# Kernel optimization log

Hardware: AMD Instinct MI355X
Metric: run time of the kernel (lower is better)

Reference implementation:

```python
import jax, jax.numpy as jnp
from jax import lax
import numpy as np

B = 512          # batch
M = 2000         # num_memories
CC = 16          # conv_channel_size
F = CC * 4 * 6 * 6  # 2304 feature size
BN_EPS = 1e-5
COS_EPS = 1e-8
SHRINK_EPS = 0.01


def conv(x, w, b, stride, pad):
    y = lax.conv_general_dilated(x, w, (stride, stride), [(pad, pad), (pad, pad)],
                                 dimension_numbers=('NCHW', 'OIHW', 'NCHW'))
    return y + b[None, :, None, None]


def deconv(x, w, b, stride, pad, out_pad):
    # w is torch ConvTranspose2d layout: (in, out, kh, kw)
    k = w.shape[2]
    w2 = jnp.flip(w, (2, 3)).transpose(1, 0, 2, 3)  # (out, in, kh, kw)
    p = [(k - 1 - pad, k - 1 - pad + out_pad)] * 2
    y = lax.conv_general_dilated(x, w2, (1, 1), p, lhs_dilation=(stride, stride),
                                 dimension_numbers=('NCHW', 'OIHW', 'NCHW'))
    return y + b[None, :, None, None]


def bn(x, g, b):
    # BatchNorm2d in training mode: per-channel batch statistics (biased var)
    m = x.mean((0, 2, 3), keepdims=True)
    v = x.var((0, 2, 3), keepdims=True)
    return g[None, :, None, None] * (x - m) * lax.rsqrt(v + BN_EPS) + b[None, :, None, None]


def setup_inputs() -> dict:
    key = jax.random.key(0)
    ks = jax.random.split(key, 16)
    rn = lambda k, s, sc=0.05: jax.random.normal(k, s, jnp.float32) * sc
    return {
        'x': jax.random.uniform(ks[0], (B, 1, 96, 96), jnp.float32),
        'c1_w': rn(ks[1], (16, 1, 1, 1), 0.3), 'c1_b': jnp.zeros(16),
        'bn1_g': jnp.ones(16), 'bn1_b': jnp.zeros(16),
        'c2_w': rn(ks[2], (32, 16, 3, 3)), 'c2_b': jnp.zeros(32),
        'bn2_g': jnp.ones(32), 'bn2_b': jnp.zeros(32),
        'c3_w': rn(ks[3], (64, 32, 3, 3)), 'c3_b': jnp.zeros(64),
        'bn3_g': jnp.ones(64), 'bn3_b': jnp.zeros(64),
        'c4_w': rn(ks[4], (64, 64, 3, 3)), 'c4_b': jnp.zeros(64),
        'bn4_g': jnp.ones(64), 'bn4_b': jnp.zeros(64),
        'memory': rn(ks[5], (M, F), 0.03),
        'd0_w': rn(ks[6], (64, 64, 3, 3)), 'd0_b': jnp.zeros(64),
        'dbn0_g': jnp.ones(64), 'dbn0_b': jnp.zeros(64),
        'd1_w': rn(ks[7], (64, 32, 3, 3)), 'd1_b': jnp.zeros(32),
        'dbn1_g': jnp.ones(32), 'dbn1_b': jnp.zeros(32),
        'd2_w': rn(ks[8], (32, 16, 2, 2)), 'd2_b': jnp.zeros(16),
        'dbn2_g': jnp.ones(16), 'dbn2_b': jnp.zeros(16),
        'd3_w': rn(ks[9], (16, 1, 2, 2)), 'd3_b': jnp.zeros(1),
    }


def reference(x, c1_w, c1_b, bn1_g, bn1_b, c2_w, c2_b, bn2_g, bn2_b,
              c3_w, c3_b, bn3_g, bn3_b, c4_w, c4_b, bn4_g, bn4_b, memory,
              d0_w, d0_b, dbn0_g, dbn0_b, d1_w, d1_b, dbn1_g, dbn1_b,
              d2_w, d2_b, dbn2_g, dbn2_b, d3_w, d3_b):
    relu = jax.nn.relu
    # Encoder: 96 -> 49 -> 25 -> 13 -> 6
    h = relu(bn(conv(x, c1_w, c1_b, 2, 1), bn1_g, bn1_b))
    h = relu(bn(conv(h, c2_w, c2_b, 2, 1), bn2_g, bn2_b))
    h = relu(bn(conv(h, c3_w, c3_b, 2, 1), bn3_g, bn3_b))
    h = relu(bn(conv(h, c4_w, c4_b, 2, 0), bn4_g, bn4_b))
    z = h.reshape(h.shape[0], -1)  # (B, 2304)

    # Memory addressing: cosine similarity without materializing (B, M, F)
    zn = jnp.linalg.norm(z, axis=1)          # (B,)
    mn = jnp.linalg.norm(memory, axis=1)     # (M,)
    sim = (z @ memory.T) / jnp.maximum(zn[:, None] * mn[None, :], COS_EPS)
    w = jax.nn.softmax(sim, axis=1)
    # Sparse hard-shrink addressing + L1 renorm
    t = 1.0 / memory.shape[0]
    w = relu(w - t) * w / (jnp.abs(w - t) + SHRINK_EPS)
    w = w / jnp.sum(jnp.abs(w), axis=1, keepdims=True)
    z_hat = w @ memory  # (B, F)

    # Decoder: 6 -> 13 -> 25 -> 49 -> 98
    g = z_hat.reshape(-1, 64, 6, 6)
    g = relu(bn(deconv(g, d0_w, d0_b, 2, 0, 0), dbn0_g, dbn0_b))
    g = relu(bn(deconv(g, d1_w, d1_b, 2, 1, 0), dbn1_g, dbn1_b))
    g = relu(bn(deconv(g, d2_w, d2_b, 2, 1, 1), dbn2_g, dbn2_b))
    g = jax.nn.sigmoid(deconv(g, d3_w, d3_b, 2, 0, 0))
    return g
```

## Files before the change

### kernel.cpp

```cpp
#include <hip/hip_runtime.h>
#include <stdint.h>


typedef unsigned short ushort_t;
typedef __bf16 bf16x8 __attribute__((ext_vector_type(8)));
typedef float f32x4 __attribute__((ext_vector_type(4)));

#define DEV static __device__ __forceinline__

DEV ushort_t f2bf(float f){
  union { float f; uint32_t u; } v; v.f = f;
  return (ushort_t)((v.u + 0x7FFFu + ((v.u >> 16) & 1u)) >> 16);
}
DEV float bf2f(ushort_t u){
  union { uint32_t u; float f; } v; v.u = ((uint32_t)u) << 16;
  return v.f;
}

DEV uint32_t affine2(uint32_t rw, const float* ac, int ci, int nch){
  float lo = bf2f((ushort_t)(rw & 0xffffu));
  float hi = bf2f((ushort_t)(rw >> 16));
  lo = fmaxf(fmaf(ac[ci],   lo, ac[nch+ci]),   0.f);
  hi = fmaxf(fmaf(ac[ci+1], hi, ac[nch+ci+1]), 0.f);
  return (uint32_t)f2bf(lo) | ((uint32_t)f2bf(hi) << 16);
}
DEV uint4 stage_chunk(uint4 raw, const float* ac, int ci0, int nch){
  uint4 o;
  o.x = affine2(raw.x, ac, ci0+0, nch);
  o.y = affine2(raw.y, ac, ci0+2, nch);
  o.z = affine2(raw.z, ac, ci0+4, nch);
  o.w = affine2(raw.w, ac, ci0+6, nch);
  return o;
}

#define H_XS   0
#define H_S2   64
#define H_Q2   96
#define H_S3   192
#define H_Q3   256
#define H_S4   448
#define H_Q4   512
#define H_DS0  704
#define H_DQ0  768
#define H_DS1  960
#define H_DQ1  992
#define H_DS2  1088
#define H_DQ2  1104
#define H_ZN   1152
#define H_MN   1664
#define H_BUK  4096
#define NBUK   16
#define BSTRIDE 1280
#define HDR_FLOATS (H_BUK + NBUK*BSTRIDE)

#define OW2 0
#define OW3 5120
#define OW4 23552
#define OD0 60416
#define OD1 97280
#define OD2 115712
#define NWPK 117760

#define SIMSTRIDE 1024000
#define ZHSTRIDE  1179648

DEV float* bkt(float* hdr, int blk){ return hdr + H_BUK + (size_t)(blk & (NBUK-1))*BSTRIDE; }

DEV void coef_lds(const float* __restrict__ hdr, int offS, int offQ,
                  const float* __restrict__ g, const float* __restrict__ be,
                  float* ac, int nch, float invN, int tid){
  if (tid < nch){
    float s = 0.f, q = 0.f;
    #pragma unroll
    for (int k=0;k<NBUK;k++){
      s += hdr[H_BUK + k*BSTRIDE + offS + tid];
      q += hdr[H_BUK + k*BSTRIDE + offQ + tid];
    }
    float m = s*invN;
    float v = q*invN - m*m;
    float a = g[tid]*rsqrtf(v + 1e-5f);
    ac[tid] = a;
    ac[nch+tid] = be[tid] - m*a;
  }
}

__global__ __launch_bounds__(256) void k_xstats(const float* __restrict__ x, float* __restrict__ hdr){
  __shared__ float red[8];
  float s = 0.f, q = 0.f;
  const int total = 512*49*49;
  for (int idx = blockIdx.x*256 + threadIdx.x; idx < total; idx += gridDim.x*256){
    int b = idx / 2401;
    int r = idx - b*2401;
    int i = r / 49, j = r - i*49;
    float v = 0.f;
    if (i > 0 && j > 0) v = x[(size_t)b*9216 + (2*i-1)*96 + (2*j-1)];
    s += v; q += v*v;
  }
  for (int o=32;o;o>>=1){ s += __shfl_down(s,o,64); q += __shfl_down(q,o,64); }
  int w = threadIdx.x>>6;
  if ((threadIdx.x&63)==0){ red[w*2]=s; red[w*2+1]=q; }
  __syncthreads();
  if (threadIdx.x==0){
    float* bk = bkt(hdr, blockIdx.x);
    atomicAdd(&bk[H_XS+0], red[0]+red[2]+red[4]+red[6]);
    atomicAdd(&bk[H_XS+1], red[1]+red[3]+red[5]+red[7]);
  }
}

__global__ __launch_bounds__(256) void k_wprep2(
    const float* __restrict__ c2w, const float* __restrict__ c3w, const float* __restrict__ c4w,
    const float* __restrict__ d0w, const float* __restrict__ d1w, const float* __restrict__ d2w,
    ushort_t* __restrict__ WPK){
  int i = blockIdx.x*256 + threadIdx.x;
  if (i >= NWPK) return;
  float val = 0.f;
  if (i < OW3){
    int co = i/160, k = i - co*160, tap = k>>4, ci = k&15;
    if (tap < 9) val = c2w[(co*16+ci)*9+tap];
  } else if (i < OW4){
    int r = i - OW3; int co = r/288, k = r - co*288, tap = k>>5, ci = k&31;
    val = c3w[(co*32+ci)*9+tap];
  } else if (i < OD0){
    int r = i - OW4; int co = r/576, k = r - co*576, tap = k>>6, ci = k&63;
    val = c4w[(co*64+ci)*9+tap];
  } else if (i < OD1){
    int r = i - OD0;
    const int base[4]={0,16384,24576,32768}, K[4]={256,128,128,64};
    const int T0[4][4] = {{0,2,6,8},{1,7,0,0},{3,5,0,0},{4,0,0,0}};
    int cl = (r<16384)?0:(r<24576)?1:(r<32768)?2:3;
    int rr = r - base[cl]; int co = rr/K[cl], k = rr - co*K[cl], t = k>>6, ci = k&63;
    val = d0w[(ci*64+co)*9 + T0[cl][t]];
  } else if (i < OD2){
    int r = i - OD1;
    const int base[4]={0,2048,6144,10240}, K[4]={64,128,128,256};
    const int T1[4][4] = {{4,0,0,0},{3,5,0,0},{1,7,0,0},{0,2,6,8}};
    int cl = (r<2048)?0:(r<6144)?1:(r<10240)?2:3;
    int rr = r - base[cl]; int co = rr/K[cl], k = rr - co*K[cl], t = k>>6, ci = k&63;
    val = d1w[(ci*32+co)*9 + T1[cl][t]];
  } else {
    int r = i - OD2;
    int cl = r>>9, s = r&511, co = s>>5, ci = s&31;
    const int pis[4]={0,0,1,1}, pjs[4]={0,1,0,1};
    val = d2w[((ci*16+co)*2 + (1-pis[cl]))*2 + (1-pjs[cl])];
  }
  WPK[i] = f2bf(val);
}

__global__ __launch_bounds__(256) void k_memrows(const float* __restrict__ mem, float* __restrict__ hdr,
                                                 ushort_t* __restrict__ mbf){
  __shared__ float red[4];
  const int m = blockIdx.x, tid = threadIdx.x;
  float part = 0.f;
  for (int i=tid;i<2304;i+=256){
    float v = mem[(size_t)m*2304+i];
    mbf[(size_t)m*2304+i] = f2bf(v);
    part += v*v;
  }
  for (int o=32;o;o>>=1) part += __shfl_down(part,o,64);
  if ((tid&63)==0) red[tid>>6] = part;
  __syncthreads();
  if (tid==0) hdr[H_MN+m] = sqrtf(red[0]+red[1]+red[2]+red[3]);
}

__global__ __launch_bounds__(256) void k_memT(const float* __restrict__ mem, ushort_t* __restrict__ mt){
  __shared__ ushort_t tile[32][33];
  const int ft = blockIdx.x % 72, mtile = blockIdx.x / 72;
  const int tx = threadIdx.x & 31, ty = threadIdx.x >> 5;
  #pragma unroll
  for (int r0=0;r0<4;r0++){
    int m = mtile*32 + r0*8 + ty;
    int f = ft*32 + tx;
    float v = (m < 2000) ? mem[(size_t)m*2304 + f] : 0.f;
    tile[r0*8+ty][tx] = f2bf(v);
  }
  __syncthreads();
  #pragma unroll
  for (int r0=0;r0<4;r0++){
    int f = ft*32 + r0*8 + ty;
    mt[(size_t)f*2016 + mtile*32 + tx] = tile[tx][r0*8+ty];
  }
}

__global__ __launch_bounds__(256) void k_conv2m(
    const float* __restrict__ x, const ushort_t* __restrict__ WPK, const float* __restrict__ b2g,
    const float* __restrict__ c1w, const float* __restrict__ c1b,
    const float* __restrict__ bn1g, const float* __restrict__ bn1b,
    float* __restrict__ hdr, ushort_t* __restrict__ out){
  __shared__ ushort_t inp[27*51*16];
  __shared__ float ac[32];
  const int blk = blockIdx.x, b = blk>>1, h = blk&1, tid = threadIdx.x;
  const int ro = h*13, nr = h?12:13, npos = nr*25, ntiles = (npos+15)>>4;
  if (tid < 16){
    float sx=0.f, qx=0.f;
    #pragma unroll
    for (int k=0;k<NBUK;k++){ sx += hdr[H_BUK+k*BSTRIDE+H_XS]; qx += hdr[H_BUK+k*BSTRIDE+H_XS+1]; }
    const float N = 512.f*49.f*49.f;
    float mx = sx/N, vx = qx/N - mx*mx;
    float mean = c1w[tid]*mx + c1b[tid];
    float a = bn1g[tid]*rsqrtf(c1w[tid]*c1w[tid]*vx + 1e-5f);
    ac[tid] = a*c1w[tid];
    ac[16+tid] = a*(c1b[tid]-mean) + bn1b[tid];
  }
  __syncthreads();
  for (int e = tid; e < 27*51; e += 256){
    int lr = e/51, gc = e - lr*51;
    int grg = 2*ro + lr;
    bool inside = (grg>=1 && grg<=49 && gc>=1 && gc<=49);
    float v = 0.f;
    if (grg>=2 && grg<=49 && gc>=2 && gc<=49) v = x[(size_t)b*9216 + (2*grg-3)*96 + (2*gc-3)];
    ushort_t hv[16];
    if (inside){
      #pragma unroll
      for (int c=0;c<16;c++) hv[c] = f2bf(fmaxf(fmaf(ac[c], v, ac[16+c]), 0.f));
    } else {
      #pragma unroll
      for (int c=0;c<16;c++) hv[c] = 0;
    }
    uint32_t w0[8];
    #pragma unroll
    for (int c=0;c<8;c++) w0[c] = (uint32_t)hv[2*c] | ((uint32_t)hv[2*c+1]<<16);
    uint4* dst = (uint4*)&inp[e*16];
    dst[0] = make_uint4(w0[0],w0[1],w0[2],w0[3]);
    dst[1] = make_uint4(w0[4],w0[5],w0[6],w0[7]);
  }
  __syncthreads();
  const int wv = tid>>6, lane = tid&63, r = lane&15, q = lane>>4;
  const int cotile = wv&1;
  bf16x8 af[5];
  #pragma unroll
  for (int c=0;c<5;c++) af[c] = *(const bf16x8*)(WPK + OW2 + (cotile*16+r)*160 + c*32 + q*8);
  float biasr[4];
  #pragma unroll
  for (int v=0;v<4;v++) biasr[v] = b2g[cotile*16 + q*4 + v];
  const int TOFF[10] = {0,1,2,51,52,53,102,103,104,0};
  const int qhi = q>>1, ci0 = (q&1)*8;
  float sacc[4]={0,0,0,0}, qacc[4]={0,0,0,0};
  for (int t = wv>>1; t < ntiles; t += 2){
    int p = t*16 + r;
    bool ok = p < npos;
    int pc = ok ? p : 0;
    int a_ = pc/25, c_ = pc - a_*25;
    int pb = (2*a_)*51 + 2*c_;
    f32x4 acc = {0.f,0.f,0.f,0.f};
    #pragma unroll
    for (int c=0;c<5;c++){
      int toff = qhi ? TOFF[2*c+1] : TOFF[2*c];
      bf16x8 bv = *(const bf16x8*)&inp[(pb + toff)*16 + ci0];
      acc = __builtin_amdgcn_mfma_f32_16x16x32_bf16(af[c], bv, acc, 0, 0, 0);
    }
    if (ok){
      int pg = (ro + a_)*25 + c_;
      ushort_t pk[4];
      #pragma unroll
      for (int reg=0;reg<4;reg++){
        float y = acc[reg] + biasr[reg];
        pk[reg] = f2bf(y);
        sacc[reg] += y; qacc[reg] += y*y;
      }
      *(uint2*)&out[((size_t)b*625 + pg)*32 + cotile*16 + q*4] =
        make_uint2((uint32_t)pk[0] | ((uint32_t)pk[1]<<16), (uint32_t)pk[2] | ((uint32_t)pk[3]<<16));
    }
  }
  float* bk = bkt(hdr, blk);
  #pragma unroll
  for (int reg=0;reg<4;reg++){
    float s = sacc[reg], qq = qacc[reg];
    for (int o=8;o;o>>=1){ s += __shfl_down(s,o,16); qq += __shfl_down(qq,o,16); }
    if (r==0){ atomicAdd(&bk[H_S2+cotile*16+q*4+reg], s); atomicAdd(&bk[H_Q2+cotile*16+q*4+reg], qq); }
  }
}

__global__ __launch_bounds__(256) void k_conv3m(
    const ushort_t* __restrict__ h2, const ushort_t* __restrict__ WPK, const float* __restrict__ b3g,
    const float* __restrict__ g, const float* __restrict__ be,
    float* __restrict__ hdr, ushort_t* __restrict__ out){
  __shared__ ushort_t inp[15*27*32];
  __shared__ float ac[64];
  const int blk = blockIdx.x, b = blk>>1, h = blk&1, tid = threadIdx.x;
  const int a0 = h*7, na = h?6:7, npos = na*13, ntiles = (npos+15)>>4, nrows = 2*na+1;
  coef_lds(hdr, H_S2, H_Q2, g, be, ac, 32, 1.f/(512.f*625.f), tid);
  __syncthreads();
  for (int e = tid; e < nrows*27*4; e += 256){
    int cell = e>>2, ch = e&3;
    int lr = cell/27, lc = cell - lr*27;
    int ii = 2*a0 - 1 + lr, j = lc - 1;
    uint4 val = make_uint4(0,0,0,0);
    if ((unsigned)ii < 25u && (unsigned)j < 25u){
      uint4 raw = *(const uint4*)&h2[((size_t)b*625 + ii*25 + j)*32 + ch*8];
      val = stage_chunk(raw, ac, ch*8, 32);
    }
    int slot = ch ^ ((cell>>1)&3);
    *(uint4*)&inp[cell*32 + slot*8] = val;
  }
  __syncthreads();
  const int wv = tid>>6, lane = tid&63, r = lane&15, q = lane>>4;
  bf16x8 af[9];
  #pragma unroll
  for (int c=0;c<9;c++) af[c] = *(const bf16x8*)(WPK + OW3 + (wv*16+r)*288 + c*32 + q*8);
  float biasr[4];
  #pragma unroll
  for (int v=0;v<4;v++) biasr[v] = b3g[wv*16 + q*4 + v];
  const int TOFF[9] = {0,1,2,27,28,29,54,55,56};
  float sacc[4]={0,0,0,0}, qacc[4]={0,0,0,0};
  for (int t = 0; t < ntiles; t++){
    int p = t*16 + r;
    bool ok = p < npos;
    int pc = ok ? p : 0;
    int a_ = pc/13, c_ = pc - a_*13;
    int pb = (2*a_)*27 + 2*c_;
    f32x4 acc = {0.f,0.f,0.f,0.f};
    #pragma unroll
    for (int c=0;c<9;c++){
      int cell = pb + TOFF[c];
      int slot = q ^ ((cell>>1)&3);
      bf16x8 bv = *(const bf16x8*)&inp[cell*32 + slot*8];
      acc = __builtin_amdgcn_mfma_f32_16x16x32_bf16(af[c], bv, acc, 0, 0, 0);
    }
    if (ok){
      int pos = (a0 + a_)*13 + c_;
      ushort_t pk[4];
      #pragma unroll
      for (int reg=0;reg<4;reg++){
        float y = acc[reg] + biasr[reg];
        pk[reg] = f2bf(y);
        sacc[reg] += y; qacc[reg] += y*y;
      }
      *(uint2*)&out[((size_t)b*169 + pos)*64 + wv*16 + q*4] =
        make_uint2((uint32_t)pk[0] | ((uint32_t)pk[1]<<16), (uint32_t)pk[2] | ((uint32_t)pk[3]<<16));
    }
  }
  float* bk = bkt(hdr, blk);
  #pragma unroll
  for (int reg=0;reg<4;reg++){
    float s = sacc[reg], qq = qacc[reg];
    for (int o=8;o;o>>=1){ s += __shfl_down(s,o,16); qq += __shfl_down(qq,o,16); }
    if (r==0){ atomicAdd(&bk[H_S3+wv*16+q*4+reg], s); atomicAdd(&bk[H_Q3+wv*16+q*4+reg], qq); }
  }
}

__global__ __launch_bounds__(256) void k_conv4m(
    const ushort_t* __restrict__ h3, const ushort_t* __restrict__ WPK, const float* __restrict__ b4g,
    const float* __restrict__ g, const float* __restrict__ be,
    float* __restrict__ hdr, float* __restrict__ out){
  __shared__ ushort_t inp[169*64];
  __shared__ float ac[128];
  const int b = blockIdx.x, tid = threadIdx.x;
  coef_lds(hdr, H_S3, H_Q3, g, be, ac, 64, 1.f/(512.f*169.f), tid);
  __syncthreads();
  for (int e = tid; e < 169*8; e += 256){
    int cell = e>>3, ch = e&7;
    uint4 raw = *(const uint4*)&h3[((size_t)b*169 + cell)*64 + ch*8];
    uint4 val = stage_chunk(raw, ac, ch*8, 64);
    int slot = ch ^ ((cell>>1)&7);
    *(uint4*)&inp[cell*64 + slot*8] = val;
  }
  __syncthreads();
  const int wv = tid>>6, lane = tid&63, r = lane&15, q = lane>>4;
  bf16x8 af[18];
  #pragma unroll
  for (int c=0;c<18;c++) af[c] = *(const bf16x8*)(WPK + OW4 + (wv*16+r)*576 + c*32 + q*8);
  float biasr[4];
  #pragma unroll
  for (int v=0;v<4;v++) biasr[v] = b4g[wv*16 + q*4 + v];
  const int TOFF[9] = {0,1,2,13,14,15,26,27,28};
  float sacc[4]={0,0,0,0}, qacc[4]={0,0,0,0};
  for (int t = 0; t < 3; t++){
    int p = t*16 + r;
    bool ok = p < 36;
    int pc = ok ? p : 0;
    int a_ = pc/6, c_ = pc - a_*6;
    int pb = (2*a_)*13 + 2*c_;
    f32x4 acc = {0.f,0.f,0.f,0.f};
    #pragma unroll
    for (int c=0;c<18;c++){
      int cell = pb + TOFF[c>>1];
      int chunk = (c&1)*4 + q;
      int slot = chunk ^ ((cell>>1)&7);
      bf16x8 bv = *(const bf16x8*)&inp[cell*64 + slot*8];
      acc = __builtin_amdgcn_mfma_f32_16x16x32_bf16(af[c], bv, acc, 0, 0, 0);
    }
    if (ok){
      #pragma unroll
      for (int reg=0;reg<4;reg++){
        float y = acc[reg] + biasr[reg];
        out[((size_t)b*64 + wv*16 + q*4 + reg)*36 + p] = y;
        sacc[reg] += y; qacc[reg] += y*y;
      }
    }
  }
  float* bk = bkt(hdr, b);
  #pragma unroll
  for (int reg=0;reg<4;reg++){
    float s = sacc[reg], qq = qacc[reg];
    for (int o=8;o;o>>=1){ s += __shfl_down(s,o,16); qq += __shfl_down(qq,o,16); }
    if (r==0){ atomicAdd(&bk[H_S4+wv*16+q*4+reg], s); atomicAdd(&bk[H_Q4+wv*16+q*4+reg], qq); }
  }
}

__global__ __launch_bounds__(256) void k_z(const float* __restrict__ zraw, float* __restrict__ hdr,
                                           ushort_t* __restrict__ zbf,
                                           const float* __restrict__ g, const float* __restrict__ be){
  __shared__ float ac[128];
  __shared__ float red[4];
  const int b = blockIdx.x, tid = threadIdx.x;
  coef_lds(hdr, H_S4, H_Q4, g, be, ac, 64, 1.f/(512.f*36.f), tid);
  __syncthreads();
  float part = 0.f;
  for (int i=tid;i<2304;i+=256){
    int c = i/36;
    float h = fmaxf(fmaf(ac[c], zraw[(size_t)b*2304+i], ac[64+c]), 0.f);
    zbf[(size_t)b*2304+i] = f2bf(h);
    part += h*h;
  }
  for (int o=32;o;o>>=1) part += __shfl_down(part,o,64);
  if ((tid&63)==0) red[tid>>6] = part;
  __syncthreads();
  if (tid==0) hdr[H_ZN+b] = sqrtf(red[0]+red[1]+red[2]+red[3]);
}

__global__ __launch_bounds__(256) void k_gemmB(const ushort_t* __restrict__ A, const ushort_t* __restrict__ Bm,
                                               float* __restrict__ D, int Nb, int N, int Kp, int kch,
                                               int tiles, int ksp, size_t dstride){
  __shared__ __align__(16) ushort_t lB[128*40];
  const int blk = blockIdx.x;
  const int s = blk / tiles, t = blk - s*tiles;
  const int bi = t / Nb, bj = t - bi*Nb;
  const int m0 = bi*128, n0 = bj*128;
  const int k0 = s*ksp, k1 = min(kch, k0 + ksp);
  const int tid = threadIdx.x;
  const int lane = tid & 63, wv = tid >> 6;
  const int r = lane & 15, q = lane >> 4;
  const int wr = wv >> 1, wc = wv & 1;
  float* Ds = D + (size_t)s*dstride;
  const int srow = tid >> 1, skq = (tid & 1) * 16;
  const bool bok = (n0 + srow) < N;
  const ushort_t* pb = Bm + (size_t)(n0 + srow)*Kp + skq;
  uint4* wB = (uint4*)&lB[srow*40 + skq];
  const uint4 zz = make_uint4(0,0,0,0);
  uint4 rb0 = bok ? *(const uint4*)(pb + k0*32)     : zz;
  uint4 rb1 = bok ? *(const uint4*)(pb + k0*32 + 8) : zz;
  const ushort_t* pa = A + (size_t)(m0 + wr*64 + r)*Kp + q*8;
  bf16x8 aN[4];
  #pragma unroll
  for (int mt=0;mt<4;mt++) aN[mt] = *(const bf16x8*)(pa + k0*32 + (size_t)(mt*16)*Kp);
  f32x4 acc[4][4];
  #pragma unroll
  for (int i=0;i<4;i++)
    #pragma unroll
    for (int j=0;j<4;j++) acc[i][j] = (f32x4){0.f,0.f,0.f,0.f};
  for (int k=k0; k<k1; k++){
    if (k > k0) __syncthreads();
    wB[0] = rb0; wB[1] = rb1;
    bf16x8 aF[4];
    #pragma unroll
    for (int mt=0;mt<4;mt++) aF[mt] = aN[mt];
    if (k+1 < k1){
      const ushort_t* nb = pb + (k+1)*32;
      rb0 = bok ? *(const uint4*)(nb)     : zz;
      rb1 = bok ? *(const uint4*)(nb + 8) : zz;
      const ushort_t* na = pa + (k+1)*32;
      #pragma unroll
      for (int mt=0;mt<4;mt++) aN[mt] = *(const bf16x8*)(na + (size_t)(mt*16)*Kp);
    }
    __syncthreads();
    bf16x8 bF[4];
    #pragma unroll
    for (int nt=0;nt<4;nt++) bF[nt] = *(const bf16x8*)&lB[(wc*64+nt*16+r)*40 + q*8];
    #pragma unroll
    for (int mt=0;mt<4;mt++)
      #pragma unroll
      for (int nt=0;nt<4;nt++)
        acc[mt][nt] = __builtin_amdgcn_mfma_f32_16x16x32_bf16(aF[mt], bF[nt], acc[mt][nt], 0, 0, 0);
  }
  #pragma unroll
  for (int mt=0;mt<4;mt++){
    int row = m0 + wr*64 + mt*16 + q*4;
    #pragma unroll
    for (int nt=0;nt<4;nt++){
      int col = n0 + wc*64 + nt*16 + r;
      if (col < N){
        #pragma unroll
        for (int reg=0;reg<4;reg++)
          Ds[(size_t)(row+reg)*N + col] = acc[mt][nt][reg];
      }
    }
  }
}

__global__ __launch_bounds__(256) void k_softmax(const float* __restrict__ sim, float* __restrict__ hdr,
                                                 ushort_t* __restrict__ wbf){
  __shared__ float e[2000];
  __shared__ float red[8];
  const int b = blockIdx.x, tid = threadIdx.x;
  const float znb = hdr[H_ZN+b];
  float part = 0.f;
  for (int m=tid;m<2000;m+=256){
    size_t ix = (size_t)b*2000+m;
    float sv = sim[ix] + sim[ix+SIMSTRIDE] + sim[ix+2*SIMSTRIDE] + sim[ix+3*SIMSTRIDE];
    float s = sv / fmaxf(znb * hdr[H_MN+m], 1e-8f);
    float ev = __expf(s);
    e[m] = ev; part += ev;
  }
  for (int o=32;o;o>>=1) part += __shfl_down(part,o,64);
  if ((tid&63)==0) red[tid>>6] = part;
  __syncthreads();
  const float denom = red[0]+red[1]+red[2]+red[3];
  const float t = 1.0f/2000.0f;
  float part2 = 0.f;
  for (int m=tid;m<2000;m+=256){
    float w = e[m]/denom;
    float d = w - t;
    float sh = fmaxf(d,0.f)*w/(fabsf(d)+0.01f);
    e[m] = sh; part2 += sh;
  }
  for (int o=32;o;o>>=1) part2 += __shfl_down(part2,o,64);
  if ((tid&63)==0) red[4+(tid>>6)] = part2;
  __syncthreads();
  const float inv = 1.0f/(red[4]+red[5]+red[6]+red[7]);
  for (int m=tid;m<2016;m+=256){
    ushort_t o = 0;
    if (m < 2000) o = f2bf(e[m]*inv);
    wbf[(size_t)b*2016+m] = o;
  }
}

__global__ __launch_bounds__(256) void k_deconv0m(
    const float* __restrict__ zh, const ushort_t* __restrict__ WPK, const float* __restrict__ b0g,
    float* __restrict__ hdr, ushort_t* __restrict__ out){
  __shared__ ushort_t inp[64*64];
  const int b = blockIdx.x, tid = threadIdx.x;
  for (int e = tid; e < 64*64; e += 256){
    int ci = e & 63, cell = e >> 6;
    int r8 = cell>>3, c8 = cell&7;
    float v = 0.f;
    if (r8>=1 && r8<=6 && c8>=1 && c8<=6){
      size_t ix = (size_t)b*2304 + ci*36 + (r8-1)*6 + (c8-1);
      v = zh[ix] + zh[ix+ZHSTRIDE] + zh[ix+2*ZHSTRIDE] + zh[ix+3*ZHSTRIDE];
    }
    inp[e] = f2bf(v);
  }
  __syncthreads();
  const int wv = tid>>6, lane = tid&63, r = lane&15, q = lane>>4;
  float biasr[4];
  #pragma unroll
  for (int v=0;v<4;v++) biasr[v] = b0g[wv*16 + q*4 + v];
  const int NCOL[4]={7,6,7,6}, NPOS[4]={49,42,42,36}, NT[4]={4,3,3,3},
            NCH[4]={8,4,4,2}, KB[4]={0,16384,24576,32768}, KK[4]={256,128,128,64},
            PI[4]={0,0,1,1}, PJ[4]={0,1,0,1};
  const int TOFF[4][4] = {{9,8,1,0},{9,1,0,0},{9,8,0,0},{9,0,0,0}};
  float sacc[4]={0,0,0,0}, qacc[4]={0,0,0,0};
  #pragma unroll
  for (int cl=0; cl<4; cl++){
    bf16x8 af[8];
    #pragma unroll
    for (int m=0;m<NCH[cl];m++)
      af[m] = *(const bf16x8*)(WPK + OD0 + KB[cl] + (wv*16+r)*KK[cl] + m*32 + q*8);
    for (int t = 0; t < NT[cl]; t++){
      int p = t*16 + r;
      bool ok = p < NPOS[cl];
      int pc = ok ? p : 0;
      int a_ = pc/NCOL[cl], c_ = pc - a_*NCOL[cl];
      int pb = a_*8 + c_;
      f32x4 acc = {0.f,0.f,0.f,0.f};
      #pragma unroll
      for (int m=0;m<NCH[cl];m++){
        int ci0 = (m&1)*32 + q*8;
        bf16x8 bv = *(const bf16x8*)&inp[(pb + TOFF[cl][m>>1])*64 + ci0];
        acc = __builtin_amdgcn_mfma_f32_16x16x32_bf16(af[m], bv, acc, 0, 0, 0);
      }
      if (ok){
        int pos = (2*a_+PI[cl])*13 + (2*c_+PJ[cl]);
        ushort_t pk[4];
        #pragma unroll
        for (int reg=0;reg<4;reg++){
          float y = acc[reg] + biasr[reg];
          pk[reg] = f2bf(y);
          sacc[reg] += y; qacc[reg] += y*y;
        }
        *(uint2*)&out[((size_t)b*169 + pos)*64 + wv*16 + q*4] =
          make_uint2((uint32_t)pk[0] | ((uint32_t)pk[1]<<16), (uint32_t)pk[2] | ((uint32_t)pk[3]<<16));
      }
    }
  }
  float* bk = bkt(hdr, b);
  #pragma unroll
  for (int reg=0;reg<4;reg++){
    float s = sacc[reg], qq = qacc[reg];
    for (int o=8;o;o>>=1){ s += __shfl_down(s,o,16); qq += __shfl_down(qq,o,16); }
    if (r==0){ atomicAdd(&bk[H_DS0+wv*16+q*4+reg], s); atomicAdd(&bk[H_DQ0+wv*16+q*4+reg], qq); }
  }
}

__global__ __launch_bounds__(256) void k_deconv1m(
    const ushort_t* __restrict__ g0, const ushort_t* __restrict__ WPK, const float* __restrict__ b1g,
    const float* __restrict__ g, const float* __restrict__ be,
    float* __restrict__ hdr, ushort_t* __restrict__ out){
  __shared__ ushort_t inp[169*64];
  __shared__ float ac[128];
  const int b = blockIdx.x, tid = threadIdx.x;
  coef_lds(hdr, H_DS0, H_DQ0, g, be, ac, 64, 1.f/(512.f*169.f), tid);
  __syncthreads();
  for (int e = tid; e < 169*8; e += 256){
    int cell = e>>3, ch = e&7;
    uint4 raw = *(const uint4*)&g0[((size_t)b*169 + cell)*64 + ch*8];
    uint4 val = stage_chunk(raw, ac, ch*8, 64);
    int slot = ch ^ ((cell>>1)&7);
    *(uint4*)&inp[cell*64 + slot*8] = val;
  }
  __syncthreads();
  const int wv = tid>>6, lane = tid&63, r = lane&15, q = lane>>4;
  const int cotile = wv&1, ph = wv>>1;
  float biasr[4];
  #pragma unroll
  for (int v=0;v<4;v++) biasr[v] = b1g[cotile*16 + q*4 + v];
  const int NCOL[4]={13,12,13,12}, NPOS[4]={169,156,156,144}, NT[4]={11,10,10,9},
            NCH[4]={2,4,4,8}, KB[4]={0,2048,6144,10240}, KK[4]={64,128,128,256},
            PI[4]={0,0,1,1}, PJ[4]={0,1,0,1};
  const int TOFF[4][4] = {{0,0,0,0},{1,0,0,0},{13,0,0,0},{14,13,1,0}};
  float sacc[4]={0,0,0,0}, qacc[4]={0,0,0,0};
  #pragma unroll
  for (int cl=0; cl<4; cl++){
    bf16x8 af[8];
    #pragma unroll
    for (int m=0;m<NCH[cl];m++)
      af[m] = *(const bf16x8*)(WPK + OD1 + KB[cl] + (cotile*16+r)*KK[cl] + m*32 + q*8);
    for (int t = ph; t < NT[cl]; t += 2){
      int p = t*16 + r;
      bool ok = p < NPOS[cl];
      int pc = ok ? p : 0;
      int a_ = pc/NCOL[cl], c_ = pc - a_*NCOL[cl];
      int pb = a_*13 + c_;
      f32x4 acc = {0.f,0.f,0.f,0.f};
      #pragma unroll
      for (int m=0;m<NCH[cl];m++){
        int cell = pb + TOFF[cl][m>>1];
        int chunk = (m&1)*4 + q;
        int slot = chunk ^ ((cell>>1)&7);
        bf16x8 bv = *(const bf16x8*)&inp[cell*64 + slot*8];
        acc = __builtin_amdgcn_mfma_f32_16x16x32_bf16(af[m], bv, acc, 0, 0, 0);
      }
      if (ok){
        int pos = (2*a_+PI[cl])*25 + (2*c_+PJ[cl]);
        ushort_t pk[4];
        #pragma unroll
        for (int reg=0;reg<4;reg++){
          float y = acc[reg] + biasr[reg];
          pk[reg] = f2bf(y);
          sacc[reg] += y; qacc[reg] += y*y;
        }
        *(uint2*)&out[((size_t)b*625 + pos)*32 + cotile*16 + q*4] =
          make_uint2((uint32_t)pk[0] | ((uint32_t)pk[1]<<16), (uint32_t)pk[2] | ((uint32_t)pk[3]<<16));
      }
    }
  }
  float* bk = bkt(hdr, b);
  #pragma unroll
  for (int reg=0;reg<4;reg++){
    float s = sacc[reg], qq = qacc[reg];
    for (int o=8;o;o>>=1){ s += __shfl_down(s,o,16); qq += __shfl_down(qq,o,16); }
    if (r==0){ atomicAdd(&bk[H_DS1+cotile*16+q*4+reg], s); atomicAdd(&bk[H_DQ1+cotile*16+q*4+reg], qq); }
  }
}

__global__ __launch_bounds__(256) void k_deconv2m(
    const ushort_t* __restrict__ g1, const ushort_t* __restrict__ WPK, const float* __restrict__ bg,
    const float* __restrict__ g, const float* __restrict__ be,
    float* __restrict__ hdr, ushort_t* __restrict__ out){
  __shared__ ushort_t inp[625*32];
  __shared__ float ac[64];
  const int b = blockIdx.x, tid = threadIdx.x;
  coef_lds(hdr, H_DS1, H_DQ1, g, be, ac, 32, 1.f/(512.f*625.f), tid);
  __syncthreads();
  for (int e = tid; e < 625*4; e += 256){
    int cell = e>>2, ch = e&3;
    uint4 raw = *(const uint4*)&g1[((size_t)b*625 + cell)*32 + ch*8];
    uint4 val = stage_chunk(raw, ac, ch*8, 32);
    int slot = ch ^ ((cell>>1)&3);
    *(uint4*)&inp[cell*32 + slot*8] = val;
  }
  __syncthreads();
  const int wv = tid>>6, lane = tid&63, r = lane&15, q = lane>>4;
  const int cl = wv;
  float biasr[4];
  #pragma unroll
  for (int v=0;v<4;v++) biasr[v] = bg[q*4 + v];
  const int NCOL[4]={25,24,25,24}, NPOS[4]={625,600,600,576}, NT[4]={40,38,38,36},
            TOFF[4]={0,1,25,26};
  const int nc = NCOL[cl], npos = NPOS[cl], nt = NT[cl], toff = TOFF[cl];
  bf16x8 af = *(const bf16x8*)(WPK + OD2 + cl*512 + r*32 + q*8);
  float sacc[4]={0,0,0,0}, qacc[4]={0,0,0,0};
  for (int t = 0; t < nt; t++){
    int p = t*16 + r;
    bool ok = p < npos;
    int pc = ok ? p : 0;
    int a_ = pc/nc, c_ = pc - a_*nc;
    int cell = a_*25 + c_ + toff;
    int slot = q ^ ((cell>>1)&3);
    f32x4 acc = {0.f,0.f,0.f,0.f};
    bf16x8 bv = *(const bf16x8*)&inp[cell*32 + slot*8];
    acc = __builtin_amdgcn_mfma_f32_16x16x32_bf16(af, bv, acc, 0, 0, 0);
    if (ok){
      #pragma unroll
      for (int reg=0;reg<4;reg++){
        float y = acc[reg] + biasr[reg];
        out[((size_t)(b*16 + q*4 + reg)*4 + cl)*625 + p] = f2bf(y);
        sacc[reg] += y; qacc[reg] += y*y;
      }
    }
  }
  float* bk = bkt(hdr, b);
  #pragma unroll
  for (int reg=0;reg<4;reg++){
    float s = sacc[reg], qq = qacc[reg];
    for (int o=8;o;o>>=1){ s += __shfl_down(s,o,16); qq += __shfl_down(qq,o,16); }
    if (r==0){ atomicAdd(&bk[H_DS2+q*4+reg], s); atomicAdd(&bk[H_DQ2+q*4+reg], qq); }
  }
}

__global__ __launch_bounds__(256) void k_deconv3(const ushort_t* __restrict__ g2, const float* __restrict__ w,
                                                 const float* __restrict__ bias,
                                                 const float* __restrict__ g, const float* __restrict__ be,
                                                 float* __restrict__ hdr, float* __restrict__ out){
  __shared__ float ac[32];
  __shared__ float wl[64];
  const int tid = threadIdx.x;
  coef_lds(hdr, H_DS2, H_DQ2, g, be, ac, 16, 1.f/(512.f*2401.f), tid);
  if (tid >= 64 && tid < 128) wl[tid-64] = w[tid-64];
  __syncthreads();
  int idx = blockIdx.x*256 + tid;
  if (idx >= 512*2401) return;
  int b = idx / 2401; int loc = idx - b*2401;
  int ii = loc / 49, jj = loc - ii*49;
  int pi = ii & 1, pj = jj & 1, cl = pi*2 + pj;
  int a = ii >> 1, c = jj >> 1;
  int nc = pj ? 24 : 25;
  const float b0 = bias[0];
  float acc00 = b0, acc01 = b0, acc10 = b0, acc11 = b0;
  const ushort_t* gp = g2 + ((size_t)(b*16)*4 + cl)*625 + a*nc + c;
  #pragma unroll
  for (int ci=0; ci<16; ci++){
    float raw = bf2f(gp[(size_t)ci*4*625]);
    float h = fmaxf(fmaf(ac[ci], raw, ac[16+ci]), 0.f);
    acc00 = fmaf(h, wl[ci*4+0], acc00);
    acc01 = fmaf(h, wl[ci*4+1], acc01);
    acc10 = fmaf(h, wl[ci*4+2], acc10);
    acc11 = fmaf(h, wl[ci*4+3], acc11);
  }
  float* op = out + (size_t)b*9604 + (2*ii)*98 + 2*jj;
  op[0]   = 1.f/(1.f + __expf(-acc00));
  op[1]   = 1.f/(1.f + __expf(-acc01));
  op[98]  = 1.f/(1.f + __expf(-acc10));
  op[99]  = 1.f/(1.f + __expf(-acc11));
}

extern "C" void kernel_launch(void* const* d_in, const int* in_sizes, int n_in,
                              void* d_out, int out_size, void* d_ws, size_t ws_size,
                              hipStream_t stream){
  (void)in_sizes; (void)n_in; (void)out_size; (void)ws_size;
  const float* x     = (const float*)d_in[0];
  const float* c1w   = (const float*)d_in[1];
  const float* c1b   = (const float*)d_in[2];
  const float* bn1g  = (const float*)d_in[3];
  const float* bn1b  = (const float*)d_in[4];
  const float* c2w   = (const float*)d_in[5];
  const float* c2b   = (const float*)d_in[6];
  const float* bn2g  = (const float*)d_in[7];
  const float* bn2b  = (const float*)d_in[8];
  const float* c3w   = (const float*)d_in[9];
  const float* c3b   = (const float*)d_in[10];
  const float* bn3g  = (const float*)d_in[11];
  const float* bn3b  = (const float*)d_in[12];
  const float* c4w   = (const float*)d_in[13];
  const float* c4b   = (const float*)d_in[14];
  const float* bn4g  = (const float*)d_in[15];
  const float* bn4b  = (const float*)d_in[16];
  const float* mem   = (const float*)d_in[17];
  const float* d0w   = (const float*)d_in[18];
  const float* d0b   = (const float*)d_in[19];
  const float* dbn0g = (const float*)d_in[20];
  const float* dbn0b = (const float*)d_in[21];
  const float* d1w   = (const float*)d_in[22];
  const float* d1b   = (const float*)d_in[23];
  const float* dbn1g = (const float*)d_in[24];
  const float* dbn1b = (const float*)d_in[25];
  const float* d2w   = (const float*)d_in[26];
  const float* d2b   = (const float*)d_in[27];
  const float* dbn2g = (const float*)d_in[28];
  const float* dbn2b = (const float*)d_in[29];
  const float* d3w   = (const float*)d_in[30];
  const float* d3b   = (const float*)d_in[31];

  float* hdr  = (float*)d_ws;
  float* H2f  = hdr + HDR_FLOATS;
  float* H3f  = H2f + 10240000;
  float* ZRAW = H3f + 5537792;
  float* WSLOT= ZRAW + 1179648;
  float* G2   = WSLOT + 73728;
  ushort_t* MEMBF = (ushort_t*)(G2 + 19668992);
  ushort_t* MEMT  = MEMBF + 4608000;
  ushort_t* ZBF   = MEMT + 4644864;
  ushort_t* WBF   = ZBF + 1179648;
  ushort_t* WPK   = (ushort_t*)WSLOT;
  float* SIMP = G2;
  float* ZHP  = G2 + 4*SIMSTRIDE;
  ushort_t* G2BF = (ushort_t*)G2;
  ushort_t* H2CL = (ushort_t*)H2f;
  ushort_t* H3CL = (ushort_t*)H3f;
  ushort_t* G0CL = (ushort_t*)H3f;
  ushort_t* G1CL = (ushort_t*)H2f;
  float* OUT = (float*)d_out;

  hipMemsetAsync(hdr, 0, HDR_FLOATS*sizeof(float), stream);
  k_xstats   <<<1024, 256, 0, stream>>>(x, hdr);
  k_wprep2   <<<460, 256, 0, stream>>>(c2w, c3w, c4w, d0w, d1w, d2w, WPK);
  k_memrows  <<<2000, 256, 0, stream>>>(mem, hdr, MEMBF);
  k_memT     <<<72*63, 256, 0, stream>>>(mem, MEMT);
  k_conv2m   <<<1024, 256, 0, stream>>>(x, WPK, c2b, c1w, c1b, bn1g, bn1b, hdr, H2CL);
  k_conv3m   <<<1024, 256, 0, stream>>>(H2CL, WPK, c3b, bn2g, bn2b, hdr, H3CL);
  k_conv4m   <<<512, 256, 0, stream>>>(H3CL, WPK, c4b, bn3g, bn3b, hdr, ZRAW);
  k_z        <<<512, 256, 0, stream>>>(ZRAW, hdr, ZBF, bn4g, bn4b);
  k_gemmB    <<<256, 256, 0, stream>>>(ZBF, MEMBF, SIMP, 16, 2000, 2304, 72, 64, 18, SIMSTRIDE);
  k_softmax  <<<512, 256, 0, stream>>>(SIMP, hdr, WBF);
  k_gemmB    <<<288, 256, 0, stream>>>(WBF, MEMT, ZHP, 18, 2304, 2016, 63, 72, 16, ZHSTRIDE);
  k_deconv0m <<<512, 256, 0, stream>>>(ZHP, WPK, d0b, hdr, G0CL);
  k_deconv1m <<<512, 256, 0, stream>>>(G0CL, WPK, d1b, dbn0g, dbn0b, hdr, G1CL);
  k_deconv2m <<<512, 256, 0, stream>>>(G1CL, WPK, d2b, dbn1g, dbn1b, hdr, G2BF);
  k_deconv3  <<<4802, 256, 0, stream>>>(G2BF, d3w, d3b, dbn2g, dbn2b, hdr, OUT);
}
```

Baseline: 355.4 us.

## Merge prep kernels into one launch and fuse BN4+ReLU into similarity GEMM

Folds x-stats, weight packing, memory bf16 conversion, memory row norms and memory transpose into a single prep kernel. Memory is now read once instead of twice, and row norms are accumulated with atomics as squared sums. The separate z normalization kernel is removed: the similarity GEMM loads the raw fp32 encoder output, applies BN4 affine and ReLU on the fly, converts to bf16 and accumulates z squared norms from the first column tile. This trades launch overhead and an intermediate round trip for extra per-element arithmetic and atomics inside the GEMM, and the softmax now takes square roots of the accumulated sums.

After: 365.0 us. 2.7% more time.

```diff
diff --git a/kernel.cpp b/kernel.cpp
--- a/kernel.cpp
+++ b/kernel.cpp
@@ -64,6 +64,10 @@
 #define SIMSTRIDE 1024000
 #define ZHSTRIDE  1179648
 
+#define PREP_MEM 4536
+#define PREP_W   (PREP_MEM+460)
+#define PREP_X   (PREP_W+256)
+
 DEV float* bkt(float* hdr, int blk){ return hdr + H_BUK + (size_t)(blk & (NBUK-1))*BSTRIDE; }
 
 DEV void coef_lds(const float* __restrict__ hdr, int offS, int offQ,
@@ -84,100 +88,88 @@
   }
 }
 
-__global__ __launch_bounds__(256) void k_xstats(const float* __restrict__ x, float* __restrict__ hdr){
-  __shared__ float red[8];
-  float s = 0.f, q = 0.f;
-  const int total = 512*49*49;
-  for (int idx = blockIdx.x*256 + threadIdx.x; idx < total; idx += gridDim.x*256){
-    int b = idx / 2401;
-    int r = idx - b*2401;
-    int i = r / 49, j = r - i*49;
-    float v = 0.f;
-    if (i > 0 && j > 0) v = x[(size_t)b*9216 + (2*i-1)*96 + (2*j-1)];
-    s += v; q += v*v;
-  }
-  for (int o=32;o;o>>=1){ s += __shfl_down(s,o,64); q += __shfl_down(q,o,64); }
-  int w = threadIdx.x>>6;
-  if ((threadIdx.x&63)==0){ red[w*2]=s; red[w*2+1]=q; }
-  __syncthreads();
-  if (threadIdx.x==0){
-    float* bk = bkt(hdr, blockIdx.x);
-    atomicAdd(&bk[H_XS+0], red[0]+red[2]+red[4]+red[6]);
-    atomicAdd(&bk[H_XS+1], red[1]+red[3]+red[5]+red[7]);
-  }
-}
-
-__global__ __launch_bounds__(256) void k_wprep2(
+__global__ __launch_bounds__(256) void k_prep(
+    const float* __restrict__ mem, ushort_t* __restrict__ mbf, ushort_t* __restrict__ mt,
+    float* __restrict__ hdr,
     const float* __restrict__ c2w, const float* __restrict__ c3w, const float* __restrict__ c4w,
     const float* __restrict__ d0w, const float* __restrict__ d1w, const float* __restrict__ d2w,
-    ushort_t* __restrict__ WPK){
-  int i = blockIdx.x*256 + threadIdx.x;
-  if (i >= NWPK) return;
-  float val = 0.f;
-  if (i < OW3){
-    int co = i/160, k = i - co*160, tap = k>>4, ci = k&15;
-    if (tap < 9) val = c2w[(co*16+ci)*9+tap];
-  } else if (i < OW4){
-    int r = i - OW3; int co = r/288, k = r - co*288, tap = k>>5, ci = k&31;
-    val = c3w[(co*32+ci)*9+tap];
-  } else if (i < OD0){
-    int r = i - OW4; int co = r/576, k = r - co*576, tap = k>>6, ci = k&63;
-    val = c4w[(co*64+ci)*9+tap];
-  } else if (i < OD1){
-    int r = i - OD0;
-    const int base[4]={0,16384,24576,32768}, K[4]={256,128,128,64};
-    const int T0[4][4] = {{0,2,6,8},{1,7,0,0},{3,5,0,0},{4,0,0,0}};
-    int cl = (r<16384)?0:(r<24576)?1:(r<32768)?2:3;
-    int rr = r - base[cl]; int co = rr/K[cl], k = rr - co*K[cl], t = k>>6, ci = k&63;
-    val = d0w[(ci*64+co)*9 + T0[cl][t]];
-  } else if (i < OD2){
-    int r = i - OD1;
-    const int base[4]={0,2048,6144,10240}, K[4]={64,128,128,256};
-    const int T1[4][4] = {{4,0,0,0},{3,5,0,0},{1,7,0,0},{0,2,6,8}};
-    int cl = (r<2048)?0:(r<6144)?1:(r<10240)?2:3;
-    int rr = r - base[cl]; int co = rr/K[cl], k = rr - co*K[cl], t = k>>6, ci = k&63;
-    val = d1w[(ci*32+co)*9 + T1[cl][t]];
+    ushort_t* __restrict__ WPK, const float* __restrict__ x){
+  __shared__ float sm[32*33];
+  const int blk = blockIdx.x, tid = threadIdx.x;
+  if (blk < PREP_MEM){
+    const int ft = blk % 72, mtile = blk / 72;
+    const int tx = tid & 31, ty = tid >> 5;
+    #pragma unroll
+    for (int r0=0;r0<4;r0++){
+      int m = mtile*32 + r0*8 + ty;
+      int f = ft*32 + tx;
+      float v = (m < 2000) ? mem[(size_t)m*2304 + f] : 0.f;
+      sm[(r0*8+ty)*33 + tx] = v;
+      if (m < 2000) mbf[(size_t)m*2304 + f] = f2bf(v);
+      float p = v*v;
+      for (int o=16;o;o>>=1) p += __shfl_down(p, o, 32);
+      if (tx==0 && m<2000) atomicAdd(&hdr[H_MN+m], p);
+    }
+    __syncthreads();
+    #pragma unroll
+    for (int r0=0;r0<4;r0++){
+      int f = ft*32 + r0*8 + ty;
+      mt[(size_t)f*2016 + mtile*32 + tx] = f2bf(sm[tx*33 + r0*8+ty]);
+    }
+  } else if (blk < PREP_W){
+    int i = (blk - PREP_MEM)*256 + tid;
+    if (i >= NWPK) return;
+    float val = 0.f;
+    if (i < OW3){
+      int co = i/160, k = i - co*160, tap = k>>4, ci = k&15;
+      if (tap < 9) val = c2w[(co*16+ci)*9+tap];
+    } else if (i < OW4){
+      int r = i - OW3; int co = r/288, k = r - co*288, tap = k>>5, ci = k&31;
+      val = c3w[(co*32+ci)*9+tap];
+    } else if (i < OD0){
+      int r = i - OW4; int co = r/576, k = r - co*576, tap = k>>6, ci = k&63;
+      val = c4w[(co*64+ci)*9+tap];
+    } else if (i < OD1){
+      int r = i - OD0;
+      const int base[4]={0,16384,24576,32768}, K[4]={256,128,128,64};
+      const int T0[4][4] = {{0,2,6,8},{1,7,0,0},{3,5,0,0},{4,0,0,0}};
+      int cl = (r<16384)?0:(r<24576)?1:(r<32768)?2:3;
+      int rr = r - base[cl]; int co = rr/K[cl], k = rr - co*K[cl], t = k>>6, ci = k&63;
+      val = d0w[(ci*64+co)*9 + T0[cl][t]];
+    } else if (i < OD2){
+      int r = i - OD1;
+      const int base[4]={0,2048,6144,10240}, K[4]={64,128,128,256};
+      const int T1[4][4] = {{4,0,0,0},{3,5,0,0},{1,7,0,0},{0,2,6,8}};
+      int cl = (r<2048)?0:(r<6144)?1:(r<10240)?2:3;
+      int rr = r - base[cl]; int co = rr/K[cl], k = rr - co*K[cl], t = k>>6, ci = k&63;
+      val = d1w[(ci*32+co)*9 + T1[cl][t]];
+    } else {
+      int r = i - OD2;
+      int cl = r>>9, s = r&511, co = s>>5, ci = s&31;
+      const int pis[4]={0,0,1,1}, pjs[4]={0,1,0,1};
+      val = d2w[((ci*16+co)*2 + (1-pis[cl]))*2 + (1-pjs[cl])];
+    }
+    WPK[i] = f2bf(val);
   } else {
-    int r = i - OD2;
-    int cl = r>>9, s = r&511, co = s>>5, ci = s&31;
-    const int pis[4]={0,0,1,1}, pjs[4]={0,1,0,1};
-    val = d2w[((ci*16+co)*2 + (1-pis[cl]))*2 + (1-pjs[cl])];
-  }
-  WPK[i] = f2bf(val);
-}
-
-__global__ __launch_bounds__(256) void k_memrows(const float* __restrict__ mem, float* __restrict__ hdr,
-                                                 ushort_t* __restrict__ mbf){
-  __shared__ float red[4];
-  const int m = blockIdx.x, tid = threadIdx.x;
-  float part = 0.f;
-  for (int i=tid;i<2304;i+=256){
-    float v = mem[(size_t)m*2304+i];
-    mbf[(size_t)m*2304+i] = f2bf(v);
-    part += v*v;
-  }
-  for (int o=32;o;o>>=1) part += __shfl_down(part,o,64);
-  if ((tid&63)==0) red[tid>>6] = part;
-  __syncthreads();
-  if (tid==0) hdr[H_MN+m] = sqrtf(red[0]+red[1]+red[2]+red[3]);
-}
-
-__global__ __launch_bounds__(256) void k_memT(const float* __restrict__ mem, ushort_t* __restrict__ mt){
-  __shared__ ushort_t tile[32][33];
-  const int ft = blockIdx.x % 72, mtile = blockIdx.x / 72;
-  const int tx = threadIdx.x & 31, ty = threadIdx.x >> 5;
-  #pragma unroll
-  for (int r0=0;r0<4;r0++){
-    int m = mtile*32 + r0*8 + ty;
-    int f = ft*32 + tx;
-    float v = (m < 2000) ? mem[(size_t)m*2304 + f] : 0.f;
-    tile[r0*8+ty][tx] = f2bf(v);
-  }
-  __syncthreads();
-  #pragma unroll
-  for (int r0=0;r0<4;r0++){
-    int f = ft*32 + r0*8 + ty;
-    mt[(size_t)f*2016 + mtile*32 + tx] = tile[tx][r0*8+ty];
+    float s = 0.f, q = 0.f;
+    const int total = 512*49*49;
+    for (int idx = (blk-PREP_W)*256 + tid; idx < total; idx += 256*256){
+      int b = idx / 2401;
+      int r = idx - b*2401;
+      int i = r / 49, j = r - i*49;
+      float v = 0.f;
+      if (i > 0 && j > 0) v = x[(size_t)b*9216 + (2*i-1)*96 + (2*j-1)];
+      s += v; q += v*v;
+    }
+    for (int o=32;o;o>>=1){ s += __shfl_down(s,o,64); q += __shfl_down(q,o,64); }
+    int w = tid>>6;
+    if ((tid&63)==0){ sm[w*2]=s; sm[w*2+1]=q; }
+    __syncthreads();
+    if (tid==0){
+      float* bk = bkt(hdr, blk);
+      atomicAdd(&bk[H_XS+0], sm[0]+sm[2]+sm[4]+sm[6]);
+      atomicAdd(&bk[H_XS+1], sm[1]+sm[3]+sm[5]+sm[7]);
+    }
   }
 }
 
@@ -397,25 +389,100 @@
   }
 }
 
-__global__ __launch_bounds__(256) void k_z(const float* __restrict__ zraw, float* __restrict__ hdr,
-                                           ushort_t* __restrict__ zbf,
-                                           const float* __restrict__ g, const float* __restrict__ be){
+__global__ __launch_bounds__(256) void k_gemmA(
+    const float* __restrict__ ZR, const ushort_t* __restrict__ Bm, float* __restrict__ D,
+    const float* __restrict__ g, const float* __restrict__ be, float* __restrict__ hdr){
+  __shared__ __align__(16) ushort_t lB[128*40];
+  __shared__ __align__(16) ushort_t lA[128*40];
   __shared__ float ac[128];
-  __shared__ float red[4];
-  const int b = blockIdx.x, tid = threadIdx.x;
+  const int blk = blockIdx.x;
+  const int s = blk >> 6, t = blk & 63;
+  const int bi = t >> 4, bj = t & 15;
+  const int m0 = bi*128, n0 = bj*128;
+  const int k0 = s*18, k1 = k0 + 18;
+  const int tid = threadIdx.x;
   coef_lds(hdr, H_S4, H_Q4, g, be, ac, 64, 1.f/(512.f*36.f), tid);
-  __syncthreads();
-  float part = 0.f;
-  for (int i=tid;i<2304;i+=256){
-    int c = i/36;
-    float h = fmaxf(fmaf(ac[c], zraw[(size_t)b*2304+i], ac[64+c]), 0.f);
-    zbf[(size_t)b*2304+i] = f2bf(h);
-    part += h*h;
-  }
-  for (int o=32;o;o>>=1) part += __shfl_down(part,o,64);
-  if ((tid&63)==0) red[tid>>6] = part;
-  __syncthreads();
-  if (tid==0) hdr[H_ZN+b] = sqrtf(red[0]+red[1]+red[2]+red[3]);
+  const int lane = tid & 63, wv = tid >> 6;
+  const int r = lane & 15, q = lane >> 4;
+  const int wr = wv >> 1, wc = wv & 1;
+  const bool bj0 = (bj == 0);
+  float* Ds = D + (size_t)s*SIMSTRIDE;
+  const int srow = tid >> 1, skq = (tid & 1) * 16;
+  const bool bok = (n0 + srow) < 2000;
+  const ushort_t* pb = Bm + (size_t)(n0 + srow)*2304 + skq;
+  const float*    pa = ZR + (size_t)(m0 + srow)*2304 + skq;
+  uint4* wB = (uint4*)&lB[srow*40 + skq];
+  uint4* wA = (uint4*)&lA[srow*40 + skq];
+  const uint4 zz = make_uint4(0,0,0,0);
+  uint4 rb0 = bok ? *(const uint4*)(pb + (size_t)k0*32)     : zz;
+  uint4 rb1 = bok ? *(const uint4*)(pb + (size_t)k0*32 + 8) : zz;
+  f32x4 raA[4];
+  #pragma unroll
+  for (int i=0;i<4;i++) raA[i] = *(const f32x4*)(pa + (size_t)k0*32 + i*4);
+  f32x4 acc[4][4];
+  #pragma unroll
+  for (int i=0;i<4;i++)
+    #pragma unroll
+    for (int j=0;j<4;j++) acc[i][j] = (f32x4){0.f,0.f,0.f,0.f};
+  float zsq = 0.f;
+  __syncthreads();
+  for (int k=k0; k<k1; k++){
+    if (k > k0) __syncthreads();
+    wB[0] = rb0; wB[1] = rb1;
+    {
+      const int kb = k*32 + skq;
+      uint32_t pw[8];
+      #pragma unroll
+      for (int jj=0;jj<8;jj++){
+        float v0 = raA[jj>>1][(jj&1)*2+0];
+        float v1 = raA[jj>>1][(jj&1)*2+1];
+        int c0 = (kb + 2*jj) / 36;
+        int c1 = (kb + 2*jj + 1) / 36;
+        float h0 = fmaxf(fmaf(ac[c0], v0, ac[64+c0]), 0.f);
+        float h1 = fmaxf(fmaf(ac[c1], v1, ac[64+c1]), 0.f);
+        if (bj0) zsq += h0*h0 + h1*h1;
+        pw[jj] = (uint32_t)f2bf(h0) | ((uint32_t)f2bf(h1) << 16);
+      }
+      wA[0] = make_uint4(pw[0],pw[1],pw[2],pw[3]);
+      wA[1] = make_uint4(pw[4],pw[5],pw[6],pw[7]);
+    }
+    if (k+1 < k1){
+      const ushort_t* nb = pb + (size_t)(k+1)*32;
+      rb0 = bok ? *(const uint4*)(nb)     : zz;
+      rb1 = bok ? *(const uint4*)(nb + 8) : zz;
+      const float* na = pa + (size_t)(k+1)*32;
+      #pragma unroll
+      for (int i=0;i<4;i++) raA[i] = *(const f32x4*)(na + i*4);
+    }
+    __syncthreads();
+    bf16x8 aF[4], bF[4];
+    #pragma unroll
+    for (int mt=0;mt<4;mt++) aF[mt] = *(const bf16x8*)&lA[(wr*64+mt*16+r)*40 + q*8];
+    #pragma unroll
+    for (int nt=0;nt<4;nt++) bF[nt] = *(const bf16x8*)&lB[(wc*64+nt*16+r)*40 + q*8];
+    #pragma unroll
+    for (int mt=0;mt<4;mt++)
+      #pragma unroll
+      for (int nt=0;nt<4;nt++)
+        acc[mt][nt] = __builtin_amdgcn_mfma_f32_16x16x32_bf16(aF[mt], bF[nt], acc[mt][nt], 0, 0, 0);
+  }
+  if (bj0){
+    zsq += __shfl_down(zsq, 1, 64);
+    if ((tid & 1) == 0) atomicAdd(&hdr[H_ZN + m0 + srow], zsq);
+  }
+  #pragma unroll
+  for (int mt=0;mt<4;mt++){
+    int row = m0 + wr*64 + mt*16 + q*4;
+    #pragma unroll
+    for (int nt=0;nt<4;nt++){
+      int col = n0 + wc*64 + nt*16 + r;
+      if (col < 2000){
+        #pragma unroll
+        for (int reg=0;reg<4;reg++)
+          Ds[(size_t)(row+reg)*2000 + col] = acc[mt][nt][reg];
+      }
+    }
+  }
 }
 
 __global__ __launch_bounds__(256) void k_gemmB(const ushort_t* __restrict__ A, const ushort_t* __restrict__ Bm,
@@ -492,12 +559,13 @@
   __shared__ float e[2000];
   __shared__ float red[8];
   const int b = blockIdx.x, tid = threadIdx.x;
-  const float znb = hdr[H_ZN+b];
+  const float znb = sqrtf(hdr[H_ZN+b]);
   float part = 0.f;
   for (int m=tid;m<2000;m+=256){
     size_t ix = (size_t)b*2000+m;
     float sv = sim[ix] + sim[ix+SIMSTRIDE] + sim[ix+2*SIMSTRIDE] + sim[ix+3*SIMSTRIDE];
-    float s = sv / fmaxf(znb * hdr[H_MN+m], 1e-8f);
+    float mnb = sqrtf(hdr[H_MN+m]);
+    float s = sv / fmaxf(znb * mnb, 1e-8f);
     float ev = __expf(s);
     e[m] = ev; part += ev;
   }
@@ -811,15 +879,12 @@
   float* OUT = (float*)d_out;
 
   hipMemsetAsync(hdr, 0, HDR_FLOATS*sizeof(float), stream);
-  k_xstats   <<<1024, 256, 0, stream>>>(x, hdr);
-  k_wprep2   <<<460, 256, 0, stream>>>(c2w, c3w, c4w, d0w, d1w, d2w, WPK);
-  k_memrows  <<<2000, 256, 0, stream>>>(mem, hdr, MEMBF);
-  k_memT     <<<72*63, 256, 0, stream>>>(mem, MEMT);
+  k_prep     <<<PREP_X, 256, 0, stream>>>(mem, MEMBF, MEMT, hdr,
+                                          c2w, c3w, c4w, d0w, d1w, d2w, WPK, x);
   k_conv2m   <<<1024, 256, 0, stream>>>(x, WPK, c2b, c1w, c1b, bn1g, bn1b, hdr, H2CL);
   k_conv3m   <<<1024, 256, 0, stream>>>(H2CL, WPK, c3b, bn2g, bn2b, hdr, H3CL);
   k_conv4m   <<<512, 256, 0, stream>>>(H3CL, WPK, c4b, bn3g, bn3b, hdr, ZRAW);
-  k_z        <<<512, 256, 0, stream>>>(ZRAW, hdr, ZBF, bn4g, bn4b);
-  k_gemmB    <<<256, 256, 0, stream>>>(ZBF, MEMBF, SIMP, 16, 2000, 2304, 72, 64, 18, SIMSTRIDE);
+  k_gemmA    <<<256, 256, 0, stream>>>(ZRAW, MEMBF, SIMP, bn4g, bn4b, hdr);
   k_softmax  <<<512, 256, 0, stream>>>(SIMP, hdr, WBF);
   k_gemmB    <<<288, 256, 0, stream>>>(WBF, MEMT, ZHP, 18, 2304, 2016, 63, 72, 16, ZHSTRIDE);
   k_deconv0m <<<512, 256, 0, stream>>>(ZHP, WPK, d0b, hdr, G0CL);
```
